# Performance work log

Measured on AMD Instinct MI355X. Metric: run time of the kernel, lower is better.

## Reference

```python
import jax, jax.numpy as jnp
import numpy as np

N = 50000
E = 400000
IN_DIM = 256
HEADS = 4
C = 64          # out_channels per head
HC = HEADS * C  # 256
OUT_DIM = 32
NEG_SLOPE = 0.2


def setup_inputs() -> dict:
    key = jax.random.key(0)
    ks = jax.random.split(key, 16)
    s = lambda fan_in: 1.0 / np.sqrt(fan_in)
    return {
        "x": jax.random.normal(ks[0], (N, IN_DIM), jnp.float32),
        "edge_index": jax.random.randint(ks[1], (2, E), 0, N, jnp.int64),
        # conv1 (lin_l == lin_r, shared)
        "W1": jax.random.normal(ks[2], (IN_DIM, HC), jnp.float32) * s(IN_DIM),
        "b1": jnp.zeros((HC,), jnp.float32),
        "att1": jax.random.normal(ks[3], (HEADS, C), jnp.float32) * s(C),
        # conv2
        "W2": jax.random.normal(ks[4], (HC, HC), jnp.float32) * s(HC),
        "b2": jnp.zeros((HC,), jnp.float32),
        "att2": jax.random.normal(ks[5], (HEADS, C), jnp.float32) * s(C),
        # post_mp: Linear(HC, C_hidden=64) -> Linear(64, OUT_DIM)
        "Wp1": jax.random.normal(ks[6], (HC, C), jnp.float32) * s(HC),
        "bp1": jnp.zeros((C,), jnp.float32),
        "Wp2": jax.random.normal(ks[7], (C, OUT_DIM), jnp.float32) * s(C),
        "bp2": jnp.zeros((OUT_DIM,), jnp.float32),
    }


def _gatv2_layer(x, src, dst, W, b, att):
    # shared lin_l == lin_r, so x_source == x_target projection
    h = (x @ W + b).reshape(-1, HEADS, C)          # [N, H, C]
    x_j = h[src]                                    # source features per edge [E, H, C]
    x_i = h[dst]                                    # target features per edge [E, H, C]
    e = jax.nn.leaky_relu(x_i + x_j, NEG_SLOPE)     # [E, H, C]
    alpha = jnp.einsum('ehc,hc->eh', e, att)        # [E, H]
    # segment softmax grouped by target node (dst)
    amax = jax.ops.segment_max(alpha, dst, num_segments=N)   # [N, H]
    ex = jnp.exp(alpha - amax[dst])
    denom = jax.ops.segment_sum(ex, dst, num_segments=N)     # [N, H]
    alpha = ex / (denom[dst] + 1e-16)
    out = jax.ops.segment_sum(x_j * alpha[:, :, None], dst, num_segments=N)  # [N, H, C]
    return out.reshape(-1, HC)


def reference(x, edge_index, W1, b1, att1, W2, b2, att2, Wp1, bp1, Wp2, bp2):
    src, dst = edge_index[0], edge_index[1]
    h = jax.nn.relu(_gatv2_layer(x, src, dst, W1, b1, att1))
    h = jax.nn.relu(_gatv2_layer(h, src, dst, W2, b2, att2))
    out = (h @ Wp1 + bp1) @ Wp2 + bp2
    return jax.nn.sigmoid(out)
```

## Files before the change

### kernel.cpp

```cpp
#include <hip/hip_runtime.h>
#include <math.h>

#define HC 256
#define NEG_SLOPE 0.2f

typedef __attribute__((ext_vector_type(2))) _Float16 h16x2;
typedef __attribute__((ext_vector_type(4))) _Float16 h16x4;
typedef __attribute__((ext_vector_type(8))) _Float16 f16x8;
typedef __attribute__((ext_vector_type(4))) float f32x4;

__device__ __forceinline__ unsigned short f2h16(float f) {
  _Float16 x = (_Float16)f;
  return __builtin_bit_cast(unsigned short, x);
}
__device__ __forceinline__ float h2f(unsigned short u) {
  _Float16 x = __builtin_bit_cast(_Float16, u);
  return (float)x;
}

__device__ __forceinline__ int detect64(const int* e) {
  int v = e[2 * (threadIdx.x & 63) + 1];
  return (__ballot(v != 0) == 0ULL) ? 1 : 0;
}

__device__ __forceinline__ int edge_val(const void* p, int is64, long long idx) {
  return is64 ? (int)((const long long*)p)[idx] : ((const int*)p)[idx];
}

__device__ __forceinline__ int wave_incl_scan(int v) {
  int lane = threadIdx.x & 63;
#pragma unroll
  for (int off = 1; off < 64; off <<= 1) {
    int y = __shfl_up(v, off, 64);
    if (lane >= off) v += y;
  }
  return v;
}

__global__ __launch_bounds__(256) void count_prep_kernel(
    const void* __restrict__ edges, int* __restrict__ counts, int E, int CB,
    const float* __restrict__ W1, const float* __restrict__ W2,
    const float* __restrict__ Wp1, const float* __restrict__ bp1,
    const float* __restrict__ Wp2, const float* __restrict__ bp2,
    unsigned short* __restrict__ W1t, unsigned short* __restrict__ W2t,
    unsigned short* __restrict__ Wft16, float* __restrict__ bf) {
  const int b = blockIdx.x, t = threadIdx.x;
  if (b < CB) {
    int is64 = detect64((const int*)edges);
    int e = b * 256 + t;
    if (e < E) {
      int dst = edge_val(edges, is64, (long long)E + e);
      atomicAdd(&counts[dst], 1);
    }
    return;
  }
  const int pb = b - CB;
  if (pb < 512) {
    int n = pb & 255;
    const float* W = (pb >> 8) ? W2 : W1;
    unsigned short* Wt = (pb >> 8) ? W2t : W1t;
    Wt[(size_t)n * 256 + t] = f2h16(W[(size_t)t * 256 + n]);
    return;
  }
  float acc[32];
#pragma unroll
  for (int o = 0; o < 32; ++o) acc[o] = 0.f;
  for (int ll = 0; ll < 64; ++ll) {
    float w1 = Wp1[t * 64 + ll];
#pragma unroll
    for (int o = 0; o < 32; ++o) acc[o] += w1 * Wp2[ll * 32 + o];
  }
#pragma unroll
  for (int o = 0; o < 32; ++o) Wft16[o * 256 + t] = f2h16(acc[o]);
  if (t < 32) {
    float s = bp2[t];
    for (int ll = 0; ll < 64; ++ll) s += bp1[ll] * Wp2[ll * 32 + t];
    bf[t] = s;
  }
}

__global__ __launch_bounds__(1024) void scan1_kernel(const int* __restrict__ counts,
                                                     int* __restrict__ excl,
                                                     int* __restrict__ partials, int N) {
  __shared__ int wsum[16];
  int i = blockIdx.x * 1024 + threadIdx.x;
  int wid = threadIdx.x >> 6, lane = threadIdx.x & 63;
  int v = (i < N) ? counts[i] : 0;
  int incl = wave_incl_scan(v);
  if (lane == 63) wsum[wid] = incl;
  __syncthreads();
  if (wid == 0) {
    int s = (lane < 16) ? wsum[lane] : 0;
    s = wave_incl_scan(s);
    if (lane < 16) wsum[lane] = s;
  }
  __syncthreads();
  int base = (wid > 0) ? wsum[wid - 1] : 0;
  if (i < N) excl[i] = base + incl - v;
  if (threadIdx.x == 1023) partials[blockIdx.x] = base + incl;
}

__global__ void scan2_kernel(int* __restrict__ partials, int P) {
  int lane = threadIdx.x;
  if (P <= 64) {
    int v = (lane < P) ? partials[lane] : 0;
    int incl = wave_incl_scan(v);
    if (lane < P) partials[lane] = incl - v;
  } else if (lane == 0) {
    int run = 0;
    for (int i = 0; i < P; ++i) { int v = partials[i]; partials[i] = run; run += v; }
  }
}

__global__ void scan3copy_kernel(int* __restrict__ excl, const int* __restrict__ partials,
                                 int* __restrict__ cursor, int N, int E) {
  int i = blockIdx.x * blockDim.x + threadIdx.x;
  if (i < N) {
    int v = excl[i] + partials[i >> 10];
    excl[i] = v;
    cursor[i] = v;
  }
  if (i == 0) excl[N] = E;
}

template <bool AF32>
__device__ __forceinline__ void gemm_body(
    const void* __restrict__ Araw, const unsigned short* __restrict__ Bt,
    const float* __restrict__ bias, unsigned short* __restrict__ C, int M,
    int orig, int nwg) {
  __shared__ __align__(16) short As[2][128 * 64];
  __shared__ __align__(16) short Bs[2][128 * 64];
  const int q = nwg >> 3, r = nwg & 7;
  const int xcd = orig & 7, pos = orig >> 3;
  const int logical = (xcd < r ? xcd * (q + 1) : r * (q + 1) + (xcd - r) * q) + pos;
  const int m0 = (logical >> 1) * 128, n0 = (logical & 1) * 128;

  const int t = threadIdx.x;
  const int l = t & 63, w = t >> 6;
  const int wr = w >> 1, wc = w & 1;
  const int l15 = l & 15, lg = l >> 4;

  const int ccs = ((t & 7) ^ ((t >> 3) & 7)) * 8;
  int rowL[4], ldsI[4];
#pragma unroll
  for (int i = 0; i < 4; ++i) {
    rowL[i] = i * 32 + (t >> 3);
    ldsI[i] = (i * 256 + t) * 8;
  }

  f32x4 acc[4][4];
#pragma unroll
  for (int m = 0; m < 4; ++m)
#pragma unroll
    for (int n = 0; n < 4; ++n) acc[m][n] = (f32x4){0.f, 0.f, 0.f, 0.f};

  uint4 ra[4], rb[4];
  auto LOAD = [&](int ks) {
    int k0 = ks * 64;
#pragma unroll
    for (int i = 0; i < 4; ++i) {
      int ar = m0 + rowL[i];
      ar = (ar < M) ? ar : (M - 1);
      if (AF32) {
        const float* A = (const float*)Araw;
        float4 fa = *(const float4*)(A + (size_t)ar * 256 + k0 + ccs);
        float4 fb = *(const float4*)(A + (size_t)ar * 256 + k0 + ccs + 4);
        ra[i].x = f2h16(fa.x) | ((unsigned)f2h16(fa.y) << 16);
        ra[i].y = f2h16(fa.z) | ((unsigned)f2h16(fa.w) << 16);
        ra[i].z = f2h16(fb.x) | ((unsigned)f2h16(fb.y) << 16);
        ra[i].w = f2h16(fb.z) | ((unsigned)f2h16(fb.w) << 16);
      } else {
        const unsigned short* A = (const unsigned short*)Araw;
        ra[i] = *(const uint4*)(A + (size_t)ar * 256 + k0 + ccs);
      }
      rb[i] = *(const uint4*)(Bt + (size_t)(n0 + rowL[i]) * 256 + k0 + ccs);
    }
  };
  auto WRITE = [&](int buf) {
#pragma unroll
    for (int i = 0; i < 4; ++i) {
      *(uint4*)&As[buf][ldsI[i]] = ra[i];
      *(uint4*)&Bs[buf][ldsI[i]] = rb[i];
    }
  };

  int rA[4], rB[4];
#pragma unroll
  for (int m = 0; m < 4; ++m) rA[m] = (wr * 64 + m * 16 + l15) * 64;
#pragma unroll
  for (int n = 0; n < 4; ++n) rB[n] = (wc * 64 + n * 16 + l15) * 64;
  const int swz0 = ((0 * 4 + lg) ^ (l & 7)) * 8;
  const int swz1 = ((1 * 4 + lg) ^ (l & 7)) * 8;

  LOAD(0);
  WRITE(0);
  __syncthreads();
  for (int ks = 0; ks < 4; ++ks) {
    if (ks < 3) LOAD(ks + 1);
    const int buf = ks & 1;
#pragma unroll
    for (int kk = 0; kk < 2; ++kk) {
      const int swz = kk ? swz1 : swz0;
      f16x8 a[4], b[4];
#pragma unroll
      for (int m = 0; m < 4; ++m) a[m] = *(const f16x8*)&As[buf][rA[m] + swz];
#pragma unroll
      for (int n = 0; n < 4; ++n) b[n] = *(const f16x8*)&Bs[buf][rB[n] + swz];
#pragma unroll
      for (int m = 0; m < 4; ++m)
#pragma unroll
        for (int n = 0; n < 4; ++n)
          acc[m][n] = __builtin_amdgcn_mfma_f32_16x16x32_f16(a[m], b[n], acc[m][n], 0, 0, 0);
    }
    if (ks < 3) WRITE((ks + 1) & 1);
    __syncthreads();
  }

  float bcol[4];
#pragma unroll
  for (int n = 0; n < 4; ++n) bcol[n] = bias[n0 + wc * 64 + n * 16 + l15];
#pragma unroll
  for (int m = 0; m < 4; ++m) {
    int baseRow = m0 + wr * 64 + m * 16 + lg * 4;
#pragma unroll
    for (int rr = 0; rr < 4; ++rr) {
      int row = baseRow + rr;
      if (row < M) {
#pragma unroll
        for (int n = 0; n < 4; ++n)
          C[(size_t)row * 256 + n0 + wc * 64 + n * 16 + l15] = f2h16(acc[m][n][rr] + bcol[n]);
      }
    }
  }
}

__global__ __launch_bounds__(256) void gemm1_fill_kernel(
    const float* __restrict__ x, const unsigned short* __restrict__ W1t,
    const float* __restrict__ b1, unsigned short* __restrict__ h, int M, int GB,
    const void* __restrict__ edges, int* __restrict__ cursor,
    int* __restrict__ csr_src, int E) {
  if ((int)blockIdx.x < GB) {
    gemm_body<true>((const void*)x, W1t, b1, h, M, blockIdx.x, GB);
    return;
  }
  int is64 = detect64((const int*)edges);
  int e = (blockIdx.x - GB) * 256 + threadIdx.x;
  if (e >= E) return;
  int src = edge_val(edges, is64, e);
  int dst = edge_val(edges, is64, (long long)E + e);
  int p = atomicAdd(&cursor[dst], 1);
  csr_src[p] = src;
}

__global__ __launch_bounds__(256) void gemm2_kernel(
    const unsigned short* __restrict__ A, const unsigned short* __restrict__ W2t,
    const float* __restrict__ b2, unsigned short* __restrict__ h, int M) {
  gemm_body<false>((const void*)A, W2t, b2, h, M, blockIdx.x, gridDim.x);
}

__global__ __launch_bounds__(256) void gat_fused_kernel(
    const unsigned short* __restrict__ h, const float* __restrict__ att,
    const int* __restrict__ row_ptr, const int* __restrict__ csr_src,
    unsigned short* __restrict__ out16, int N) {
  const int wid = threadIdx.x >> 6, ln = threadIdx.x & 63;
  const int node = blockIdx.x * 4 + wid;
  if (node >= N) return;
  const float4 attv = *(const float4*)(att + ln * 4);
  const h16x4 at4 = {(_Float16)attv.x, (_Float16)attv.y, (_Float16)attv.z, (_Float16)attv.w};
  const _Float16 kns = (_Float16)NEG_SLOPE;
  const h16x4 k4 = {kns, kns, kns, kns};
  const h16x4 hi4 = *(const h16x4*)(h + (size_t)node * HC + ln * 4);
  const int beg = __builtin_amdgcn_readfirstlane(row_ptr[node]);
  const int end = __builtin_amdgcn_readfirstlane(row_ptr[node + 1]);
  const size_t vo = (size_t)ln * 4;

  float d = 0.f;
  float4 S = make_float4(0.f, 0.f, 0.f, 0.f);

  int e0 = beg;
  for (; e0 + 8 <= end; e0 += 8) {
    h16x4 hj[8];
    float p[8];
#pragma unroll
    for (int c = 0; c < 8; ++c) {
      int j = __builtin_amdgcn_readfirstlane(csr_src[e0 + c]);
      hj[c] = *(const h16x4*)(h + (size_t)j * HC + vo);
    }
#pragma unroll
    for (int c = 0; c < 8; ++c) {
      h16x4 s4 = hi4 + hj[c];
      h16x4 l4 = __builtin_elementwise_max(s4, s4 * k4);
      h16x4 m4 = l4 * at4;
      h16x2 a2 = m4.lo + m4.hi;
      float pp = (float)a2.x + (float)a2.y;
#pragma unroll
      for (int off = 1; off < 16; off <<= 1) pp += __shfl_xor(pp, off, 64);
      p[c] = pp;
    }
#pragma unroll
    for (int c = 0; c < 8; ++c) {
      float wgt = __expf(p[c]);
      d += wgt;
      S.x += wgt * (float)hj[c].x;
      S.y += wgt * (float)hj[c].y;
      S.z += wgt * (float)hj[c].z;
      S.w += wgt * (float)hj[c].w;
    }
  }
  if (e0 < end) {
    const int cnt = end - e0;
    h16x4 hj[8];
    float p[8];
#pragma unroll
    for (int c = 0; c < 8; ++c) {
      int j = __builtin_amdgcn_readfirstlane(csr_src[min(e0 + c, end - 1)]);
      hj[c] = *(const h16x4*)(h + (size_t)j * HC + vo);
    }
#pragma unroll
    for (int c = 0; c < 8; ++c) {
      h16x4 s4 = hi4 + hj[c];
      h16x4 l4 = __builtin_elementwise_max(s4, s4 * k4);
      h16x4 m4 = l4 * at4;
      h16x2 a2 = m4.lo + m4.hi;
      float pp = (float)a2.x + (float)a2.y;
#pragma unroll
      for (int off = 1; off < 16; off <<= 1) pp += __shfl_xor(pp, off, 64);
      p[c] = pp;
    }
#pragma unroll
    for (int c = 0; c < 8; ++c) {
      float wgt = (c < cnt) ? __expf(p[c]) : 0.f;
      d += wgt;
      S.x += wgt * (float)hj[c].x;
      S.y += wgt * (float)hj[c].y;
      S.z += wgt * (float)hj[c].z;
      S.w += wgt * (float)hj[c].w;
    }
  }

  float inv = (d > 0.f) ? (1.f / d) : 0.f;
  ushort4 ub;
  ub.x = f2h16(fmaxf(S.x * inv, 0.f));
  ub.y = f2h16(fmaxf(S.y * inv, 0.f));
  ub.z = f2h16(fmaxf(S.z * inv, 0.f));
  ub.w = f2h16(fmaxf(S.w * inv, 0.f));
  *(ushort4*)(out16 + (size_t)node * HC + vo) = ub;
}

__global__ __launch_bounds__(256) void post_kernel(
    const unsigned short* __restrict__ g, const unsigned short* __restrict__ Wft16,
    const float* __restrict__ bf, float* __restrict__ out, int M) {
  const int l = threadIdx.x & 63, w = threadIdx.x >> 6;
  const int r0 = blockIdx.x * 256 + w * 64;
  const int l15 = l & 15, lg = l >> 4;

  f16x8 bfrag[2][8];
#pragma unroll
  for (int n = 0; n < 2; ++n)
#pragma unroll
    for (int ks = 0; ks < 8; ++ks)
      bfrag[n][ks] = *(const f16x8*)(Wft16 + (size_t)(n * 16 + l15) * 256 + ks * 32 + lg * 8);

  float b0 = bf[l15], b1 = bf[16 + l15];

  f32x4 acc[4][2];
#pragma unroll
  for (int m = 0; m < 4; ++m)
#pragma unroll
    for (int n = 0; n < 2; ++n) acc[m][n] = (f32x4){0.f, 0.f, 0.f, 0.f};

#pragma unroll
  for (int m = 0; m < 4; ++m) {
    int row = r0 + m * 16 + l15;
    row = (row < M) ? row : (M - 1);
    const unsigned short* gp = g + (size_t)row * 256 + lg * 8;
#pragma unroll
    for (int ks = 0; ks < 8; ++ks) {
      f16x8 a = *(const f16x8*)(gp + ks * 32);
      acc[m][0] = __builtin_amdgcn_mfma_f32_16x16x32_f16(a, bfrag[0][ks], acc[m][0], 0, 0, 0);
      acc[m][1] = __builtin_amdgcn_mfma_f32_16x16x32_f16(a, bfrag[1][ks], acc[m][1], 0, 0, 0);
    }
  }

#pragma unroll
  for (int m = 0; m < 4; ++m) {
    int baseRow = r0 + m * 16 + lg * 4;
#pragma unroll
    for (int rr = 0; rr < 4; ++rr) {
      int row = baseRow + rr;
      if (row < M) {
        float v0 = acc[m][0][rr] + b0;
        float v1 = acc[m][1][rr] + b1;
        out[(size_t)row * 32 + l15]      = 1.f / (1.f + __expf(-v0));
        out[(size_t)row * 32 + 16 + l15] = 1.f / (1.f + __expf(-v1));
      }
    }
  }
}

extern "C" void kernel_launch(void* const* d_in, const int* in_sizes, int n_in,
                              void* d_out, int out_size, void* d_ws, size_t ws_size,
                              hipStream_t stream) {
  const float* x    = (const float*)d_in[0];
  const void*  ei   = d_in[1];
  const float* W1   = (const float*)d_in[2];
  const float* b1   = (const float*)d_in[3];
  const float* att1 = (const float*)d_in[4];
  const float* W2   = (const float*)d_in[5];
  const float* b2   = (const float*)d_in[6];
  const float* att2 = (const float*)d_in[7];
  const float* Wp1  = (const float*)d_in[8];
  const float* bp1  = (const float*)d_in[9];
  const float* Wp2  = (const float*)d_in[10];
  const float* bp2  = (const float*)d_in[11];
  const int N = in_sizes[0] / 256;
  const int E = in_sizes[1] / 2;
  float* outp = (float*)d_out;

  char* ws = (char*)d_ws;
  size_t off = 0;
  auto alloc = [&](size_t bytes) {
    char* p = ws + off;
    off = (off + bytes + 255) & ~(size_t)255;
    return p;
  };
  unsigned short* h16  = (unsigned short*)alloc((size_t)N * 256 * 2);
  unsigned short* a16  = (unsigned short*)alloc((size_t)N * 256 * 2);
  unsigned short* g16  = (unsigned short*)alloc((size_t)N * 256 * 2);
  int*   row_ptr  = (int*)alloc((size_t)(N + 1) * 4);
  int*   cursor   = (int*)alloc((size_t)N * 4);
  int*   csr      = (int*)alloc((size_t)E * 4);
  int*   partials = (int*)alloc((size_t)((N + 1023) / 1024 + 1) * 4);
  unsigned short* W1t = (unsigned short*)alloc(256 * 256 * 2);
  unsigned short* W2t = (unsigned short*)alloc(256 * 256 * 2);
  unsigned short* Wft16 = (unsigned short*)alloc(32 * 256 * 2);
  float* bfv      = (float*)alloc(32 * 4);

  const int nb = (N + 255) / 256;
  const int eb = (E + 255) / 256;
  const int P  = (N + 1023) / 1024;
  const int mt = (N + 127) / 128;
  const int GB = mt * 2;

  hipMemsetAsync(cursor, 0, (size_t)N * 4, stream);
  hipLaunchKernelGGL(count_prep_kernel, dim3(eb + 513), dim3(256), 0, stream,
                     ei, cursor, E, eb, W1, W2, Wp1, bp1, Wp2, bp2, W1t, W2t, Wft16, bfv);
  hipLaunchKernelGGL(scan1_kernel, dim3(P), dim3(1024), 0, stream, cursor, row_ptr, partials, N);
  hipLaunchKernelGGL(scan2_kernel, dim3(1), dim3(64), 0, stream, partials, P);
  hipLaunchKernelGGL(scan3copy_kernel, dim3(nb), dim3(256), 0, stream, row_ptr, partials, cursor, N, E);
  hipLaunchKernelGGL(gemm1_fill_kernel, dim3(GB + eb), dim3(256), 0, stream,
                     x, W1t, b1, h16, N, GB, ei, cursor, csr, E);
  hipLaunchKernelGGL(gat_fused_kernel, dim3((N + 3) / 4), dim3(256), 0, stream,
                     h16, att1, row_ptr, csr, a16, N);
  hipLaunchKernelGGL(gemm2_kernel, dim3(GB), dim3(256), 0, stream, a16, W2t, b2, h16, N);
  hipLaunchKernelGGL(gat_fused_kernel, dim3((N + 3) / 4), dim3(256), 0, stream,
                     h16, att2, row_ptr, csr, g16, N);
  hipLaunchKernelGGL(post_kernel, dim3((N + 255) / 256), dim3(256), 0, stream,
                     g16, Wft16, bfv, outp, N);
}
```

Baseline: 190.1 us.

## Merge scan kernels, batch edge work per block, use fdot2 for attention scores

Folds the single-block partials scan into the scan-add kernel, so each block rescans the partials into shared memory and one launch is removed. The edge-count and CSR-fill blocks now process four edges per thread, which cuts the number of blocks. The attention dot product uses packed fp16 fdot2 with fp32 accumulation instead of an fp16 multiply and add chain. The tail loop now skips padded edges entirely. It drops the P>64 fallback, so it assumes at most 64 partials (N ≤ 65536).

```diff
diff --git a/kernel.cpp b/kernel.cpp
--- a/kernel.cpp
+++ b/kernel.cpp
@@ -47,10 +47,14 @@
   const int b = blockIdx.x, t = threadIdx.x;
   if (b < CB) {
     int is64 = detect64((const int*)edges);
-    int e = b * 256 + t;
-    if (e < E) {
-      int dst = edge_val(edges, is64, (long long)E + e);
-      atomicAdd(&counts[dst], 1);
+    int base = b * 1024;
+#pragma unroll
+    for (int k = 0; k < 4; ++k) {
+      int e = base + k * 256 + t;
+      if (e < E) {
+        int dst = edge_val(edges, is64, (long long)E + e);
+        atomicAdd(&counts[dst], 1);
+      }
     }
     return;
   }
@@ -100,23 +104,20 @@
   if (threadIdx.x == 1023) partials[blockIdx.x] = base + incl;
 }
 
-__global__ void scan2_kernel(int* __restrict__ partials, int P) {
-  int lane = threadIdx.x;
-  if (P <= 64) {
-    int v = (lane < P) ? partials[lane] : 0;
+__global__ __launch_bounds__(256) void scan23_kernel(
+    int* __restrict__ excl, const int* __restrict__ partials,
+    int* __restrict__ cursor, int N, int E, int P) {
+  __shared__ int pref[64];
+  int t = threadIdx.x;
+  if (t < 64) {
+    int v = (t < P) ? partials[t] : 0;
     int incl = wave_incl_scan(v);
-    if (lane < P) partials[lane] = incl - v;
-  } else if (lane == 0) {
-    int run = 0;
-    for (int i = 0; i < P; ++i) { int v = partials[i]; partials[i] = run; run += v; }
-  }
-}
-
-__global__ void scan3copy_kernel(int* __restrict__ excl, const int* __restrict__ partials,
-                                 int* __restrict__ cursor, int N, int E) {
-  int i = blockIdx.x * blockDim.x + threadIdx.x;
+    pref[t] = incl - v;
+  }
+  __syncthreads();
+  int i = blockIdx.x * 256 + t;
   if (i < N) {
-    int v = excl[i] + partials[i >> 10];
+    int v = excl[i] + pref[i >> 10];
     excl[i] = v;
     cursor[i] = v;
   }
@@ -244,12 +245,17 @@
     return;
   }
   int is64 = detect64((const int*)edges);
-  int e = (blockIdx.x - GB) * 256 + threadIdx.x;
-  if (e >= E) return;
-  int src = edge_val(edges, is64, e);
-  int dst = edge_val(edges, is64, (long long)E + e);
-  int p = atomicAdd(&cursor[dst], 1);
-  csr_src[p] = src;
+  int base = (blockIdx.x - GB) * 1024;
+#pragma unroll
+  for (int k = 0; k < 4; ++k) {
+    int e = base + k * 256 + threadIdx.x;
+    if (e < E) {
+      int src = edge_val(edges, is64, e);
+      int dst = edge_val(edges, is64, (long long)E + e);
+      int p = atomicAdd(&cursor[dst], 1);
+      csr_src[p] = src;
+    }
+  }
 }
 
 __global__ __launch_bounds__(256) void gemm2_kernel(
@@ -266,7 +272,8 @@
   const int node = blockIdx.x * 4 + wid;
   if (node >= N) return;
   const float4 attv = *(const float4*)(att + ln * 4);
-  const h16x4 at4 = {(_Float16)attv.x, (_Float16)attv.y, (_Float16)attv.z, (_Float16)attv.w};
+  const h16x2 at_lo = {(_Float16)attv.x, (_Float16)attv.y};
+  const h16x2 at_hi = {(_Float16)attv.z, (_Float16)attv.w};
   const _Float16 kns = (_Float16)NEG_SLOPE;
   const h16x4 k4 = {kns, kns, kns, kns};
   const h16x4 hi4 = *(const h16x4*)(h + (size_t)node * HC + ln * 4);
@@ -290,9 +297,8 @@
     for (int c = 0; c < 8; ++c) {
       h16x4 s4 = hi4 + hj[c];
       h16x4 l4 = __builtin_elementwise_max(s4, s4 * k4);
-      h16x4 m4 = l4 * at4;
-      h16x2 a2 = m4.lo + m4.hi;
-      float pp = (float)a2.x + (float)a2.y;
+      float pp = __builtin_amdgcn_fdot2(l4.lo, at_lo,
+                 __builtin_amdgcn_fdot2(l4.hi, at_hi, 0.f, false), false);
 #pragma unroll
       for (int off = 1; off < 16; off <<= 1) pp += __shfl_xor(pp, off, 64);
       p[c] = pp;
@@ -310,7 +316,6 @@
   if (e0 < end) {
     const int cnt = end - e0;
     h16x4 hj[8];
-    float p[8];
 #pragma unroll
     for (int c = 0; c < 8; ++c) {
       int j = __builtin_amdgcn_readfirstlane(csr_src[min(e0 + c, end - 1)]);
@@ -318,23 +323,20 @@
     }
 #pragma unroll
     for (int c = 0; c < 8; ++c) {
-      h16x4 s4 = hi4 + hj[c];
-      h16x4 l4 = __builtin_elementwise_max(s4, s4 * k4);
-      h16x4 m4 = l4 * at4;
-      h16x2 a2 = m4.lo + m4.hi;
-      float pp = (float)a2.x + (float)a2.y;
-#pragma unroll
-      for (int off = 1; off < 16; off <<= 1) pp += __shfl_xor(pp, off, 64);
-      p[c] = pp;
-    }
-#pragma unroll
-    for (int c = 0; c < 8; ++c) {
-      float wgt = (c < cnt) ? __expf(p[c]) : 0.f;
-      d += wgt;
-      S.x += wgt * (float)hj[c].x;
-      S.y += wgt * (float)hj[c].y;
-      S.z += wgt * (float)hj[c].z;
-      S.w += wgt * (float)hj[c].w;
+      if (c < cnt) {
+        h16x4 s4 = hi4 + hj[c];
+        h16x4 l4 = __builtin_elementwise_max(s4, s4 * k4);
+        float pp = __builtin_amdgcn_fdot2(l4.lo, at_lo,
+                   __builtin_amdgcn_fdot2(l4.hi, at_hi, 0.f, false), false);
+#pragma unroll
+        for (int off = 1; off < 16; off <<= 1) pp += __shfl_xor(pp, off, 64);
+        float wgt = __expf(pp);
+        d += wgt;
+        S.x += wgt * (float)hj[c].x;
+        S.y += wgt * (float)hj[c].y;
+        S.z += wgt * (float)hj[c].z;
+        S.w += wgt * (float)hj[c].w;
+      }
     }
   }
 
@@ -436,19 +438,18 @@
   unsigned short* Wft16 = (unsigned short*)alloc(32 * 256 * 2);
   float* bfv      = (float*)alloc(32 * 4);
 
-  const int nb = (N + 255) / 256;
-  const int eb = (E + 255) / 256;
-  const int P  = (N + 1023) / 1024;
-  const int mt = (N + 127) / 128;
-  const int GB = mt * 2;
+  const int nb  = (N + 255) / 256;
+  const int P   = (N + 1023) / 1024;
+  const int CBe = (E + 1023) / 1024;
+  const int mt  = (N + 127) / 128;
+  const int GB  = mt * 2;
 
   hipMemsetAsync(cursor, 0, (size_t)N * 4, stream);
-  hipLaunchKernelGGL(count_prep_kernel, dim3(eb + 513), dim3(256), 0, stream,
-                     ei, cursor, E, eb, W1, W2, Wp1, bp1, Wp2, bp2, W1t, W2t, Wft16, bfv);
+  hipLaunchKernelGGL(count_prep_kernel, dim3(CBe + 513), dim3(256), 0, stream,
+                     ei, cursor, E, CBe, W1, W2, Wp1, bp1, Wp2, bp2, W1t, W2t, Wft16, bfv);
   hipLaunchKernelGGL(scan1_kernel, dim3(P), dim3(1024), 0, stream, cursor, row_ptr, partials, N);
-  hipLaunchKernelGGL(scan2_kernel, dim3(1), dim3(64), 0, stream, partials, P);
-  hipLaunchKernelGGL(scan3copy_kernel, dim3(nb), dim3(256), 0, stream, row_ptr, partials, cursor, N, E);
-  hipLaunchKernelGGL(gemm1_fill_kernel, dim3(GB + eb), dim3(256), 0, stream,
+  hipLaunchKernelGGL(scan23_kernel, dim3(nb), dim3(256), 0, stream, row_ptr, partials, cursor, N, E, P);
+  hipLaunchKernelGGL(gemm1_fill_kernel, dim3(GB + CBe), dim3(256), 0, stream,
                      x, W1t, b1, h16, N, GB, ei, cursor, csr, E);
   hipLaunchKernelGGL(gat_fused_kernel, dim3((N + 3) / 4), dim3(256), 0, stream,
                      h16, att1, row_ptr, csr, a16, N);
```

Measured after the change: 178.9 us. -5.9%, faster.
